# Performance work log

Hardware: AMD Instinct MI355X
Metric: run time of the kernel (lower is better)

Reference implementation:

```python
import jax, jax.numpy as jnp
import numpy as np

# Module constants (match init_kwargs)
H, W = 8, 64            # feature-map grid, N = H*W = 512
HK, WK = 7, 11          # local window (local_k)
DIM, HEADS = 256, 8
HEAD_DIM = DIM // HEADS
SCALE = HEAD_DIM ** -0.5


def _local_mask():
    # Equivalent to the original padded-ones/crop construction: position (h', w')
    # is attendable from (h, w) iff |h-h'| <= HK//2 and |w-w'| <= WK//2.
    dh = np.abs(np.arange(H)[:, None] - np.arange(H)[None, :]) <= HK // 2   # [H, H]
    dw = np.abs(np.arange(W)[:, None] - np.arange(W)[None, :]) <= WK // 2   # [W, W]
    allowed = (dh[:, None, :, None] & dw[None, :, None, :]).reshape(H * W, H * W)
    return jnp.asarray(np.where(allowed, 0.0, -np.inf), dtype=jnp.float32)  # [N, N]


def setup_inputs() -> dict:
    key = jax.random.key(0)
    k1, k2, k3, k4 = jax.random.split(key, 4)
    B, N = 64, H * W
    x = jax.random.normal(k1, (B, N, DIM), dtype=jnp.float32)
    w_qkv = jax.random.normal(k2, (3 * DIM, DIM), dtype=jnp.float32) * (DIM ** -0.5)
    w_proj = jax.random.normal(k3, (DIM, DIM), dtype=jnp.float32) * (DIM ** -0.5)
    b_proj = jax.random.normal(k4, (DIM,), dtype=jnp.float32) * 0.02
    return {"x": x, "w_qkv": w_qkv, "w_proj": w_proj, "b_proj": b_proj}


def reference(x, w_qkv, w_proj, b_proj):
    B, N, C = x.shape
    # qkv projection (no bias, qkv_bias=False)
    qkv = (x @ w_qkv.T).reshape(B, N, 3, HEADS, HEAD_DIM)
    q = qkv[:, :, 0].transpose(0, 2, 1, 3)  # [B, H, N, d]
    k = qkv[:, :, 1].transpose(0, 2, 1, 3)
    v = qkv[:, :, 2].transpose(0, 2, 1, 3)
    attn = jnp.einsum('bhnd,bhmd->bhnm', q, k) * SCALE + _local_mask()  # mask broadcasts over [B, H]
    attn = jax.nn.softmax(attn, axis=-1)  # dropout is identity (attn_drop=0)
    out = jnp.einsum('bhnm,bhmd->bhnd', attn, v)
    out = out.transpose(0, 2, 1, 3).reshape(B, N, C)
    return out @ w_proj.T + b_proj  # proj_drop=0 -> identity
```

## Files before the change

kernel.cpp:

```cpp
#include <hip/hip_runtime.h>
#include <math.h>


#define SCALE_F 0.17677669529663687f
#define GK 256
#define KC 128
#define LDB 136

typedef __attribute__((ext_vector_type(8))) short bf16x8;
typedef __attribute__((ext_vector_type(4))) float f32x4;

__device__ __forceinline__ void splitf(float a, short& hi, short& lo) {
    unsigned u = __builtin_bit_cast(unsigned, a);
    unsigned uh = u & 0xffff0000u;
    hi = (short)(uh >> 16);
    float r = a - __builtin_bit_cast(float, uh);
    unsigned ur = __builtin_bit_cast(unsigned, r);
    ur += 0x7fffu + ((ur >> 16) & 1u);
    lo = (short)(ur >> 16);
}

__global__ __launch_bounds__(256) void gemm_nt_mfma(
    const float* __restrict__ A,
    const float* __restrict__ B,
    const float* __restrict__ bias,
    float* __restrict__ C,
    int M, int N)
{
    __shared__ short Ah[64 * LDB], Al[64 * LDB], Bh[64 * LDB], Bl[64 * LDB];

    const int tid = threadIdx.x;
    const int n0 = blockIdx.x * 64;
    const int m0 = blockIdx.y * 64;

    const int wid  = tid >> 6;
    const int lane = tid & 63;
    const int fr = lane & 15;
    const int fq = lane >> 4;

    f32x4 acc[4];
#pragma unroll
    for (int nt = 0; nt < 4; ++nt) acc[nt] = (f32x4){0.f, 0.f, 0.f, 0.f};

    for (int kc = 0; kc < 2; ++kc) {
        if (kc) __syncthreads();
#pragma unroll
        for (int i = 0; i < 8; ++i) {
            const int idx = i * 256 + tid;
            const int row = idx >> 5;
            const int c4  = idx & 31;
            const float4 va = *(const float4*)(A + (size_t)(m0 + row) * GK + kc * KC + c4 * 4);
            const float4 vb = *(const float4*)(B + (size_t)(n0 + row) * GK + kc * KC + c4 * 4);
            short h0, h1, h2, h3, l0, l1, l2, l3;
            splitf(va.x, h0, l0); splitf(va.y, h1, l1);
            splitf(va.z, h2, l2); splitf(va.w, h3, l3);
            int2 ph, pl;
            ph.x = (int)(unsigned short)h0 | ((int)h1 << 16);
            ph.y = (int)(unsigned short)h2 | ((int)h3 << 16);
            pl.x = (int)(unsigned short)l0 | ((int)l1 << 16);
            pl.y = (int)(unsigned short)l2 | ((int)l3 << 16);
            *(int2*)&Ah[row * LDB + c4 * 4] = ph;
            *(int2*)&Al[row * LDB + c4 * 4] = pl;
            splitf(vb.x, h0, l0); splitf(vb.y, h1, l1);
            splitf(vb.z, h2, l2); splitf(vb.w, h3, l3);
            ph.x = (int)(unsigned short)h0 | ((int)h1 << 16);
            ph.y = (int)(unsigned short)h2 | ((int)h3 << 16);
            pl.x = (int)(unsigned short)l0 | ((int)l1 << 16);
            pl.y = (int)(unsigned short)l2 | ((int)l3 << 16);
            *(int2*)&Bh[row * LDB + c4 * 4] = ph;
            *(int2*)&Bl[row * LDB + c4 * 4] = pl;
        }
        __syncthreads();

        bf16x8 ah[4], al[4];
#pragma unroll
        for (int kt = 0; kt < 4; ++kt) {
            const int off = (wid * 16 + fr) * LDB + kt * 32 + fq * 8;
            ah[kt] = *(const bf16x8*)&Ah[off];
            al[kt] = *(const bf16x8*)&Al[off];
        }
#pragma unroll
        for (int nt = 0; nt < 4; ++nt) {
#pragma unroll
            for (int kt = 0; kt < 4; ++kt) {
                const int off = (nt * 16 + fr) * LDB + kt * 32 + fq * 8;
                const bf16x8 bh = *(const bf16x8*)&Bh[off];
                const bf16x8 bl = *(const bf16x8*)&Bl[off];
                acc[nt] = __builtin_amdgcn_mfma_f32_16x16x32_bf16(al[kt], bh, acc[nt], 0, 0, 0);
                acc[nt] = __builtin_amdgcn_mfma_f32_16x16x32_bf16(ah[kt], bl, acc[nt], 0, 0, 0);
                acc[nt] = __builtin_amdgcn_mfma_f32_16x16x32_bf16(ah[kt], bh, acc[nt], 0, 0, 0);
            }
        }
    }

#pragma unroll
    for (int nt = 0; nt < 4; ++nt) {
        const int col = n0 + nt * 16 + fr;
        const float bv = bias ? bias[col] : 0.f;
#pragma unroll
        for (int i = 0; i < 4; ++i) {
            const int row = m0 + wid * 16 + fq * 4 + i;
            C[(size_t)row * N + col] = acc[nt][i] + bv;
        }
    }
}

__global__ __launch_bounds__(512, 4) void attn_local(
    const float* __restrict__ qkv,
    float* __restrict__ attn_out)
{
    __shared__ float Kt[2][32][65];
    __shared__ float Vt[2][32][65];

    const int h = blockIdx.x;
    const int b = blockIdx.y;
    const int tid = threadIdx.x;
    const int qh = tid >> 6;
    const int w = tid & 63;

    const int sc = tid >> 3;
    const int sd = (tid & 7) * 4;

    const size_t rowbase = (size_t)b * 512 * 768;

    const float* qp = qkv + rowbase + (size_t)(qh * 64 + w) * 768 + h * 32;
    float q[32];
#pragma unroll
    for (int d4 = 0; d4 < 8; ++d4) {
        float4 v = *(const float4*)(qp + d4 * 4);
        q[d4 * 4 + 0] = v.x * SCALE_F;
        q[d4 * 4 + 1] = v.y * SCALE_F;
        q[d4 * 4 + 2] = v.z * SCALE_F;
        q[d4 * 4 + 3] = v.w * SCALE_F;
    }

    float mrun = -INFINITY, lrun = 0.f;
    float outv[32];
#pragma unroll
    for (int d = 0; d < 32; ++d) outv[d] = 0.f;

    const int r0 = (qh - 3 < 0) ? 0 : qh - 3;
    const int r1 = (qh + 3 > 7) ? 7 : qh + 3;

    {
        const float* sp = qkv + rowbase + (size_t)(sc)*768 + h * 32 + sd;
        float4 kv = *(const float4*)(sp + 256);
        float4 vv = *(const float4*)(sp + 512);
#pragma unroll
        for (int j = 0; j < 4; ++j) {
            Kt[0][sd + j][sc] = ((const float*)&kv)[j];
            Vt[0][sd + j][sc] = ((const float*)&vv)[j];
        }
    }
    __syncthreads();

    for (int r = 0; r < 8; ++r) {
        const int cur = r & 1;
        float4 kv, vv;
        if (r < 7) {
            const float* sp = qkv + rowbase + (size_t)((r + 1) * 64 + sc) * 768 + h * 32 + sd;
            kv = *(const float4*)(sp + 256);
            vv = *(const float4*)(sp + 512);
        }
        if (r >= r0 && r <= r1) {
            float p[11];
            int cc[11];
            float rowmax = -INFINITY;
#pragma unroll
            for (int dc = 0; dc < 11; ++dc) {
                const int c = w + dc - 5;
                const bool valid = (c >= 0) && (c < 64);
                const int cl = c < 0 ? 0 : (c > 63 ? 63 : c);
                cc[dc] = cl;
                float acc = 0.f;
#pragma unroll
                for (int d = 0; d < 32; ++d) acc += q[d] * Kt[cur][d][cl];
                p[dc] = valid ? acc : -INFINITY;
                rowmax = fmaxf(rowmax, p[dc]);
            }
            const float mnew = fmaxf(mrun, rowmax);
            const float scl = __expf(mrun - mnew);
            float lsum = 0.f;
#pragma unroll
            for (int dc = 0; dc < 11; ++dc) {
                p[dc] = __expf(p[dc] - mnew);
                lsum += p[dc];
            }
            lrun = lrun * scl + lsum;
#pragma unroll
            for (int d = 0; d < 32; ++d) {
                float t = 0.f;
#pragma unroll
                for (int dc = 0; dc < 11; ++dc) t += p[dc] * Vt[cur][d][cc[dc]];
                outv[d] = outv[d] * scl + t;
            }
            mrun = mnew;
        }
        if (r < 7) {
            const int nxt = cur ^ 1;
#pragma unroll
            for (int j = 0; j < 4; ++j) {
                Kt[nxt][sd + j][sc] = ((const float*)&kv)[j];
                Vt[nxt][sd + j][sc] = ((const float*)&vv)[j];
            }
        }
        __syncthreads();
    }

    const float inv = 1.f / lrun;
    float* op = attn_out + (size_t)(b * 512 + qh * 64 + w) * 256 + h * 32;
#pragma unroll
    for (int d4 = 0; d4 < 8; ++d4) {
        float4 v;
        v.x = outv[d4 * 4 + 0] * inv;
        v.y = outv[d4 * 4 + 1] * inv;
        v.z = outv[d4 * 4 + 2] * inv;
        v.w = outv[d4 * 4 + 3] * inv;
        *(float4*)(op + d4 * 4) = v;
    }
}

extern "C" void kernel_launch(void* const* d_in, const int* in_sizes, int n_in,
                              void* d_out, int out_size, void* d_ws, size_t ws_size,
                              hipStream_t stream)
{
    const float* x      = (const float*)d_in[0];
    const float* w_qkv  = (const float*)d_in[1];
    const float* w_proj = (const float*)d_in[2];
    const float* b_proj = (const float*)d_in[3];
    float* out = (float*)d_out;

    float* qkv  = (float*)d_ws;
    float* attn = qkv + (size_t)32768 * 768;

    const int M = 32768;

    gemm_nt_mfma<<<dim3(768 / 64, M / 64), 256, 0, stream>>>(x, w_qkv, nullptr, qkv, M, 768);

    attn_local<<<dim3(8, 64), 512, 0, stream>>>(qkv, attn);

    gemm_nt_mfma<<<dim3(256 / 64, M / 64), 256, 0, stream>>>(attn, w_proj, b_proj, out, M, 256);
}
```

Before: 307.3 us.

## Rewrite local attention kernel to use split-bf16 MFMA for QK and PV

Replaces the scalar per-thread local attention with a matrix-core version. QK^T scores are computed with three-term split-bf16 MFMAs on banded 16x16 tiles, masked to the 11-wide window, then an online softmax runs per tile. P·V uses MFMA with P rounded to single bf16 and V split into hi/lo parts. The goal is to cut the FP32 FMA and LDS-read cost of the scalar loops. In exchange it adds wasted work on out-of-band tile entries, cross-lane shuffles, and slight precision loss on P.

```diff
diff --git a/kernel.cpp b/kernel.cpp
--- a/kernel.cpp
+++ b/kernel.cpp
@@ -18,6 +18,12 @@
     unsigned ur = __builtin_bit_cast(unsigned, r);
     ur += 0x7fffu + ((ur >> 16) & 1u);
     lo = (short)(ur >> 16);
+}
+
+__device__ __forceinline__ unsigned short bf16rne(float x) {
+    unsigned u = __builtin_bit_cast(unsigned, x);
+    u += 0x7fffu + ((u >> 16) & 1u);
+    return (unsigned short)(u >> 16);
 }
 
 __global__ __launch_bounds__(256) void gemm_nt_mfma(
@@ -105,118 +111,237 @@
     }
 }
 
-__global__ __launch_bounds__(512, 4) void attn_local(
+__global__ __launch_bounds__(512) void attn_local_mfma(
     const float* __restrict__ qkv,
     float* __restrict__ attn_out)
 {
-    __shared__ float Kt[2][32][65];
-    __shared__ float Vt[2][32][65];
+    __shared__ __align__(16) short Kh[2][64 * 40], Kl[2][64 * 40];
+    __shared__ __align__(16) short Vh[2][32 * 72], Vl[2][32 * 72];
 
     const int h = blockIdx.x;
     const int b = blockIdx.y;
     const int tid = threadIdx.x;
     const int qh = tid >> 6;
-    const int w = tid & 63;
+    const int lane = tid & 63;
+    const int w0 = lane & 15;
+    const int g  = lane >> 4;
+    const size_t rowbase = (size_t)b * 512 * 768;
+
+    bf16x8 qfh[4], qfl[4];
+#pragma unroll
+    for (int wt = 0; wt < 4; ++wt) {
+        const float* qp = qkv + rowbase + (size_t)(qh * 64 + wt * 16 + w0) * 768 + h * 32 + g * 8;
+        const float4 qa = *(const float4*)qp;
+        const float4 qb = *(const float4*)(qp + 4);
+        float qv[8] = {qa.x, qa.y, qa.z, qa.w, qb.x, qb.y, qb.z, qb.w};
+#pragma unroll
+        for (int e = 0; e < 8; ++e) {
+            short hh, ll;
+            splitf(qv[e] * SCALE_F, hh, ll);
+            qfh[wt][e] = hh;
+            qfl[wt][e] = ll;
+        }
+    }
+
+    f32x4 pv[2][4];
+#pragma unroll
+    for (int mt = 0; mt < 2; ++mt)
+#pragma unroll
+        for (int wt = 0; wt < 4; ++wt) pv[mt][wt] = (f32x4){0.f, 0.f, 0.f, 0.f};
+    float mrun[4] = {-INFINITY, -INFINITY, -INFINITY, -INFINITY};
+    float lrun[4] = {0.f, 0.f, 0.f, 0.f};
 
     const int sc = tid >> 3;
     const int sd = (tid & 7) * 4;
 
-    const size_t rowbase = (size_t)b * 512 * 768;
-
-    const float* qp = qkv + rowbase + (size_t)(qh * 64 + w) * 768 + h * 32;
-    float q[32];
-#pragma unroll
-    for (int d4 = 0; d4 < 8; ++d4) {
-        float4 v = *(const float4*)(qp + d4 * 4);
-        q[d4 * 4 + 0] = v.x * SCALE_F;
-        q[d4 * 4 + 1] = v.y * SCALE_F;
-        q[d4 * 4 + 2] = v.z * SCALE_F;
-        q[d4 * 4 + 3] = v.w * SCALE_F;
-    }
-
-    float mrun = -INFINITY, lrun = 0.f;
-    float outv[32];
-#pragma unroll
-    for (int d = 0; d < 32; ++d) outv[d] = 0.f;
+    {
+        const float* sp = qkv + rowbase + (size_t)sc * 768 + h * 32 + sd;
+        const float4 kv = *(const float4*)(sp + 256);
+        const float4 vv = *(const float4*)(sp + 512);
+        const float kvf[4] = {kv.x, kv.y, kv.z, kv.w};
+        const float vvf[4] = {vv.x, vv.y, vv.z, vv.w};
+        short kh4[4], kl4[4];
+#pragma unroll
+        for (int j = 0; j < 4; ++j) splitf(kvf[j], kh4[j], kl4[j]);
+        int2 ph, pl;
+        ph.x = (int)(unsigned short)kh4[0] | ((int)kh4[1] << 16);
+        ph.y = (int)(unsigned short)kh4[2] | ((int)kh4[3] << 16);
+        pl.x = (int)(unsigned short)kl4[0] | ((int)kl4[1] << 16);
+        pl.y = (int)(unsigned short)kl4[2] | ((int)kl4[3] << 16);
+        *(int2*)&Kh[0][sc * 40 + sd] = ph;
+        *(int2*)&Kl[0][sc * 40 + sd] = pl;
+#pragma unroll
+        for (int j = 0; j < 4; ++j) {
+            short vh_, vl_;
+            splitf(vvf[j], vh_, vl_);
+            Vh[0][(sd + j) * 72 + sc] = vh_;
+            Vl[0][(sd + j) * 72 + sc] = vl_;
+        }
+    }
+    __syncthreads();
 
     const int r0 = (qh - 3 < 0) ? 0 : qh - 3;
     const int r1 = (qh + 3 > 7) ? 7 : qh + 3;
 
-    {
-        const float* sp = qkv + rowbase + (size_t)(sc)*768 + h * 32 + sd;
-        float4 kv = *(const float4*)(sp + 256);
-        float4 vv = *(const float4*)(sp + 512);
-#pragma unroll
-        for (int j = 0; j < 4; ++j) {
-            Kt[0][sd + j][sc] = ((const float*)&kv)[j];
-            Vt[0][sd + j][sc] = ((const float*)&vv)[j];
-        }
-    }
-    __syncthreads();
-
     for (int r = 0; r < 8; ++r) {
         const int cur = r & 1;
-        float4 kv, vv;
+        float4 kvn, vvn;
         if (r < 7) {
             const float* sp = qkv + rowbase + (size_t)((r + 1) * 64 + sc) * 768 + h * 32 + sd;
-            kv = *(const float4*)(sp + 256);
-            vv = *(const float4*)(sp + 512);
-        }
+            kvn = *(const float4*)(sp + 256);
+            vvn = *(const float4*)(sp + 512);
+        }
+
         if (r >= r0 && r <= r1) {
-            float p[11];
-            int cc[11];
-            float rowmax = -INFINITY;
-#pragma unroll
-            for (int dc = 0; dc < 11; ++dc) {
-                const int c = w + dc - 5;
-                const bool valid = (c >= 0) && (c < 64);
-                const int cl = c < 0 ? 0 : (c > 63 ? 63 : c);
-                cc[dc] = cl;
-                float acc = 0.f;
-#pragma unroll
-                for (int d = 0; d < 32; ++d) acc += q[d] * Kt[cur][d][cl];
-                p[dc] = valid ? acc : -INFINITY;
-                rowmax = fmaxf(rowmax, p[dc]);
-            }
-            const float mnew = fmaxf(mrun, rowmax);
-            const float scl = __expf(mrun - mnew);
-            float lsum = 0.f;
-#pragma unroll
-            for (int dc = 0; dc < 11; ++dc) {
-                p[dc] = __expf(p[dc] - mnew);
-                lsum += p[dc];
-            }
-            lrun = lrun * scl + lsum;
-#pragma unroll
-            for (int d = 0; d < 32; ++d) {
-                float t = 0.f;
-#pragma unroll
-                for (int dc = 0; dc < 11; ++dc) t += p[dc] * Vt[cur][d][cc[dc]];
-                outv[d] = outv[d] * scl + t;
-            }
-            mrun = mnew;
-        }
+            bf16x8 kfh[4], kfl[4];
+#pragma unroll
+            for (int rt = 0; rt < 4; ++rt) {
+                const int off = (rt * 16 + w0) * 40 + g * 8;
+                kfh[rt] = *(const bf16x8*)&Kh[cur][off];
+                kfl[rt] = *(const bf16x8*)&Kl[cur][off];
+            }
+
+            f32x4 sm[4][3];
+#pragma unroll
+            for (int wt = 0; wt < 4; ++wt) {
+#pragma unroll
+                for (int rto = 0; rto < 3; ++rto) {
+                    const int rt = wt - 1 + rto;
+                    if (rt < 0 || rt > 3) continue;
+                    f32x4 s = (f32x4){0.f, 0.f, 0.f, 0.f};
+                    s = __builtin_amdgcn_mfma_f32_16x16x32_bf16(kfl[rt], qfh[wt], s, 0, 0, 0);
+                    s = __builtin_amdgcn_mfma_f32_16x16x32_bf16(kfh[rt], qfl[wt], s, 0, 0, 0);
+                    s = __builtin_amdgcn_mfma_f32_16x16x32_bf16(kfh[rt], qfh[wt], s, 0, 0, 0);
+                    const int wq = wt * 16 + w0;
+#pragma unroll
+                    for (int i = 0; i < 4; ++i) {
+                        const int c = rt * 16 + g * 4 + i;
+                        const int d = wq - c;
+                        if (d > 5 || d < -5) s[i] = -INFINITY;
+                    }
+                    sm[wt][rto] = s;
+                }
+            }
+
+            unsigned pk2[4][3][2];
+#pragma unroll
+            for (int wt = 0; wt < 4; ++wt) {
+                float mt_ = -INFINITY;
+#pragma unroll
+                for (int rto = 0; rto < 3; ++rto) {
+                    const int rt = wt - 1 + rto;
+                    if (rt < 0 || rt > 3) continue;
+#pragma unroll
+                    for (int i = 0; i < 4; ++i) mt_ = fmaxf(mt_, sm[wt][rto][i]);
+                }
+                mt_ = fmaxf(mt_, __shfl_xor(mt_, 16));
+                mt_ = fmaxf(mt_, __shfl_xor(mt_, 32));
+                const float mnew = fmaxf(mrun[wt], mt_);
+                const float scl = __expf(mrun[wt] - mnew);
+                float ls = 0.f;
+#pragma unroll
+                for (int rto = 0; rto < 3; ++rto) {
+                    const int rt = wt - 1 + rto;
+                    if (rt < 0 || rt > 3) continue;
+#pragma unroll
+                    for (int i = 0; i < 4; ++i) {
+                        const float p = __expf(sm[wt][rto][i] - mnew);
+                        sm[wt][rto][i] = p;
+                        ls += p;
+                    }
+                }
+                ls += __shfl_xor(ls, 16);
+                ls += __shfl_xor(ls, 32);
+                lrun[wt] = lrun[wt] * scl + ls;
+                mrun[wt] = mnew;
+#pragma unroll
+                for (int mt = 0; mt < 2; ++mt)
+#pragma unroll
+                    for (int i = 0; i < 4; ++i) pv[mt][wt][i] *= scl;
+#pragma unroll
+                for (int rto = 0; rto < 3; ++rto) {
+                    const int rt = wt - 1 + rto;
+                    if (rt < 0 || rt > 3) continue;
+#pragma unroll
+                    for (int pi = 0; pi < 2; ++pi)
+                        pk2[wt][rto][pi] = (unsigned)bf16rne(sm[wt][rto][2 * pi]) |
+                                           ((unsigned)bf16rne(sm[wt][rto][2 * pi + 1]) << 16);
+                }
+            }
+
+#pragma unroll
+            for (int kt = 0; kt < 2; ++kt) {
+                bf16x8 vfh[2], vfl[2];
+#pragma unroll
+                for (int mt = 0; mt < 2; ++mt) {
+                    const int off = (mt * 16 + w0) * 72 + kt * 32 + g * 8;
+                    vfh[mt] = *(const bf16x8*)&Vh[cur][off];
+                    vfl[mt] = *(const bf16x8*)&Vl[cur][off];
+                }
+#pragma unroll
+                for (int wt = 0; wt < 4; ++wt) {
+                    const int rtlo = 2 * kt, rthi = 2 * kt + 1;
+                    const bool has_lo = (rtlo - wt <= 1) && (wt - rtlo <= 1);
+                    const bool has_hi = (rthi - wt <= 1) && (wt - rthi <= 1);
+                    if (!has_lo && !has_hi) continue;
+                    int dw[4];
+#pragma unroll
+                    for (int jd = 0; jd < 4; ++jd) {
+                        const int src = (2 * (g & 1) + (jd >> 1)) * 16 + w0;
+                        int lo = 0, hi = 0;
+                        if (has_lo) lo = __shfl((int)pk2[wt][rtlo - wt + 1][jd & 1], src);
+                        if (has_hi) hi = __shfl((int)pk2[wt][rthi - wt + 1][jd & 1], src);
+                        dw[jd] = (g < 2) ? lo : hi;
+                    }
+                    const int4 tmp = {dw[0], dw[1], dw[2], dw[3]};
+                    const bf16x8 pf = __builtin_bit_cast(bf16x8, tmp);
+#pragma unroll
+                    for (int mt = 0; mt < 2; ++mt) {
+                        pv[mt][wt] = __builtin_amdgcn_mfma_f32_16x16x32_bf16(vfh[mt], pf, pv[mt][wt], 0, 0, 0);
+                        pv[mt][wt] = __builtin_amdgcn_mfma_f32_16x16x32_bf16(vfl[mt], pf, pv[mt][wt], 0, 0, 0);
+                    }
+                }
+            }
+        }
+
         if (r < 7) {
             const int nxt = cur ^ 1;
+            const float kvf[4] = {kvn.x, kvn.y, kvn.z, kvn.w};
+            const float vvf[4] = {vvn.x, vvn.y, vvn.z, vvn.w};
+            short kh4[4], kl4[4];
+#pragma unroll
+            for (int j = 0; j < 4; ++j) splitf(kvf[j], kh4[j], kl4[j]);
+            int2 ph, pl;
+            ph.x = (int)(unsigned short)kh4[0] | ((int)kh4[1] << 16);
+            ph.y = (int)(unsigned short)kh4[2] | ((int)kh4[3] << 16);
+            pl.x = (int)(unsigned short)kl4[0] | ((int)kl4[1] << 16);
+            pl.y = (int)(unsigned short)kl4[2] | ((int)kl4[3] << 16);
+            *(int2*)&Kh[nxt][sc * 40 + sd] = ph;
+            *(int2*)&Kl[nxt][sc * 40 + sd] = pl;
 #pragma unroll
             for (int j = 0; j < 4; ++j) {
-                Kt[nxt][sd + j][sc] = ((const float*)&kv)[j];
-                Vt[nxt][sd + j][sc] = ((const float*)&vv)[j];
+                short vh_, vl_;
+                splitf(vvf[j], vh_, vl_);
+                Vh[nxt][(sd + j) * 72 + sc] = vh_;
+                Vl[nxt][(sd + j) * 72 + sc] = vl_;
             }
         }
         __syncthreads();
     }
 
-    const float inv = 1.f / lrun;
-    float* op = attn_out + (size_t)(b * 512 + qh * 64 + w) * 256 + h * 32;
-#pragma unroll
-    for (int d4 = 0; d4 < 8; ++d4) {
-        float4 v;
-        v.x = outv[d4 * 4 + 0] * inv;
-        v.y = outv[d4 * 4 + 1] * inv;
-        v.z = outv[d4 * 4 + 2] * inv;
-        v.w = outv[d4 * 4 + 3] * inv;
-        *(float4*)(op + d4 * 4) = v;
+#pragma unroll
+    for (int wt = 0; wt < 4; ++wt) {
+        const float inv = 1.f / lrun[wt];
+        float* op = attn_out + (size_t)(b * 512 + qh * 64 + wt * 16 + w0) * 256 + h * 32;
+#pragma unroll
+        for (int mt = 0; mt < 2; ++mt) {
+            float4 o;
+            o.x = pv[mt][wt][0] * inv;
+            o.y = pv[mt][wt][1] * inv;
+            o.z = pv[mt][wt][2] * inv;
+            o.w = pv[mt][wt][3] * inv;
+            *(float4*)(op + mt * 16 + g * 4) = o;
+        }
     }
 }
 
@@ -237,7 +362,7 @@
 
     gemm_nt_mfma<<<dim3(768 / 64, M / 64), 256, 0, stream>>>(x, w_qkv, nullptr, qkv, M, 768);
 
-    attn_local<<<dim3(8, 64), 512, 0, stream>>>(qkv, attn);
+    attn_local_mfma<<<dim3(8, 64), 512, 0, stream>>>(qkv, attn);
 
     gemm_nt_mfma<<<dim3(256 / 64, M / 64), 256, 0, stream>>>(attn, w_proj, b_proj, out, M, 256);
 }
```

New measurement: 276.6 us. 1.11x faster.
